# Performance work log

Hardware: AMD Instinct MI355X
Metric: run time of the kernel (lower is better)

## Reference

```python
import jax, jax.numpy as jnp
import numpy as np

D_MODEL = 1024
N_HEADS = 16
D_K = D_MODEL // N_HEADS
ROPE_BASE = 500000.0
RMS_EPS = 1e-10


def _rms_norm(x, w):
    # RMSNorm over last dim (per-head d_k): w * x / sqrt(mean(x^2) + eps)
    rms = jnp.sqrt(jnp.mean(x * x, axis=-1, keepdims=True) + RMS_EPS)
    return w * (x / rms)


def _rotate_half(x):
    x1, x2 = x[..., : x.shape[-1] // 2], x[..., x.shape[-1] // 2:]
    return jnp.concatenate([-x2, x1], axis=-1)


def _rope_cos_sin(seq_len):
    inv_freq = 1.0 / (ROPE_BASE ** (jnp.arange(0, D_K, 2, dtype=jnp.float32) / D_K))
    t = jnp.arange(seq_len, dtype=jnp.float32)
    freqs = jnp.outer(t, inv_freq)                # (S, d_k/2)
    emb = jnp.concatenate([freqs, freqs], axis=-1)  # (S, d_k)
    return jnp.cos(emb), jnp.sin(emb)


def setup_inputs() -> dict:
    key = jax.random.key(0)
    ks = jax.random.split(key, 9)
    B, S, D = 2, 2048, D_MODEL
    scale = 1.0 / np.sqrt(D)
    return {
        "q": jax.random.normal(ks[0], (B, S, D), jnp.float32),
        "k": jax.random.normal(ks[1], (B, S, D), jnp.float32),
        "v": jax.random.normal(ks[2], (B, S, D), jnp.float32),
        "w_q": jax.random.normal(ks[3], (D, D), jnp.float32) * scale,
        "w_k": jax.random.normal(ks[4], (D, D), jnp.float32) * scale,
        "w_v": jax.random.normal(ks[5], (D, D), jnp.float32) * scale,
        "w_o": jax.random.normal(ks[6], (D, D), jnp.float32) * scale,
        "q_norm_w": jnp.ones((D_K,), jnp.float32),
        "k_norm_w": jnp.ones((D_K,), jnp.float32),
    }


def reference(q, k, v, w_q, w_k, w_v, w_o, q_norm_w, k_norm_w):
    B, S, D = q.shape
    H, Dk = N_HEADS, D_K

    # QKV projections (nn.Linear without bias: x @ W.T), split into heads
    query = jnp.einsum("bsd,ed->bse", q, w_q).reshape(B, S, H, Dk).transpose(0, 2, 1, 3)
    key_ = jnp.einsum("bsd,ed->bse", k, w_k).reshape(B, S, H, Dk).transpose(0, 2, 1, 3)
    value = jnp.einsum("bsd,ed->bse", v, w_v).reshape(B, S, H, Dk).transpose(0, 2, 1, 3)

    # QK-norm (per-head RMSNorm)
    query = _rms_norm(query, q_norm_w)
    key_ = _rms_norm(key_, k_norm_w)

    # RoPE, default positions 0..S-1
    cos, sin = _rope_cos_sin(S)          # (S, d_k)
    cos = cos[None, None]                # (1,1,S,d_k)
    sin = sin[None, None]
    query = query * cos + _rotate_half(query) * sin
    key_ = key_ * cos + _rotate_half(key_) * sin

    # Causal scaled dot-product attention
    scale = 1.0 / jnp.sqrt(jnp.asarray(Dk, query.dtype))
    scores = jnp.einsum("bhqd,bhkd->bhqk", query, key_) * scale
    causal = jnp.tril(jnp.ones((S, S), dtype=bool))
    scores = jnp.where(causal, scores, jnp.finfo(scores.dtype).min)
    attn = jax.nn.softmax(scores, axis=-1)
    out = jnp.einsum("bhqk,bhkd->bhqd", attn, value)  # (B,H,S,d_k)

    out = out.transpose(0, 2, 1, 3).reshape(B, S, D)
    return jnp.einsum("bsd,ed->bse", out, w_o)
```

## Files before the change

### kernel.cpp

```cpp
#include <hip/hip_runtime.h>
#include <cstdint>
#include <cstddef>

typedef __bf16 bf16;
typedef __bf16 bf16x4_t __attribute__((ext_vector_type(4)));
typedef __bf16 bf16x8_t __attribute__((ext_vector_type(8)));
typedef float  f32x4_t  __attribute__((ext_vector_type(4)));

#define GLD_LDS16(g, l)                                                              \
  __builtin_amdgcn_global_load_lds((const __attribute__((address_space(1))) void*)(g), \
                                   (__attribute__((address_space(3))) void*)(l), 16, 0, 0)

#define S_WAITCNT_VMCNT(N) asm volatile("s_waitcnt vmcnt(" #N ")" ::: "memory")
#define S_BARRIER() asm volatile("s_barrier" ::: "memory")

__global__ __launch_bounds__(256) void cvt_kernel(
    const float* __restrict__ q, const float* __restrict__ k, const float* __restrict__ v,
    const float* __restrict__ wq, const float* __restrict__ wk, const float* __restrict__ wv,
    const float* __restrict__ wo,
    bf16* __restrict__ qb, bf16* __restrict__ kb, bf16* __restrict__ vb,
    bf16* __restrict__ wqb, bf16* __restrict__ wkb, bf16* __restrict__ wvb,
    bf16* __restrict__ wob)
{
  const float* src; bf16* dst; int n;
  switch (blockIdx.y) {
    case 0: src = q;  dst = qb;  n = 4194304; break;
    case 1: src = k;  dst = kb;  n = 4194304; break;
    case 2: src = v;  dst = vb;  n = 4194304; break;
    case 3: src = wq; dst = wqb; n = 1048576; break;
    case 4: src = wk; dst = wkb; n = 1048576; break;
    case 5: src = wv; dst = wvb; n = 1048576; break;
    default: src = wo; dst = wob; n = 1048576; break;
  }
  const int i = (blockIdx.x * 256 + threadIdx.x) * 4;
  if (i >= n) return;
  const float4 f = *(const float4*)(src + i);
  bf16x4_t o;
  o[0] = (bf16)f.x; o[1] = (bf16)f.y; o[2] = (bf16)f.z; o[3] = (bf16)f.w;
  *(bf16x4_t*)(dst + i) = o;
}

__device__ __forceinline__ void gemm_core(const bf16* __restrict__ A,
                                          const bf16* __restrict__ W,
                                          int m0, int n0, bf16* smem,
                                          f32x4_t (&acc)[4][4])
{
  const int K = 1024;
  bf16* As = smem;
  bf16* Bs = smem + 12288;
  const int t = threadIdx.x;
  const int lane = t & 63, w = t >> 6;
  const int l16 = lane & 15, qd = lane >> 4;
  const int wm = (w & 1) * 64, wn = (w >> 1) * 64;

  const int p8 = t >> 3;
  const int vslot = (t & 7) ^ (p8 & 7);
  const int srow = 2 * p8 + (vslot >> 2);
  const int scc = vslot & 3;
  const bf16* ag0 = A + (size_t)(m0 + srow) * K + scc * 8;
  const bf16* ag1 = A + (size_t)(m0 + 64 + srow) * K + scc * 8;
  const bf16* wg0 = W + (size_t)(n0 + srow) * K + scc * 8;
  const bf16* wg1 = W + (size_t)(n0 + 64 + srow) * K + scc * 8;
  const int lo0 = (w * 64) * 8;
  const int lo1 = (256 + w * 64) * 8;

  const int rslot = (((l16 & 1) * 4 + qd) ^ ((l16 >> 1) & 7)) * 8;
  const int abase = (wm >> 6) * 2048 + (l16 >> 1) * 64 + rslot;
  const int bbase = (wn >> 6) * 2048 + (l16 >> 1) * 64 + rslot;

#define STAGEG(k0_, b_)                                  \
  do {                                                   \
    GLD_LDS16(ag0 + (k0_), &As[(b_) * 4096 + lo0]);      \
    GLD_LDS16(ag1 + (k0_), &As[(b_) * 4096 + lo1]);      \
    GLD_LDS16(wg0 + (k0_), &Bs[(b_) * 4096 + lo0]);      \
    GLD_LDS16(wg1 + (k0_), &Bs[(b_) * 4096 + lo1]);      \
  } while (0)

  STAGEG(0, 0);
  STAGEG(32, 1);

  for (int k0 = 0; k0 < K; k0 += 32) {
    const int it = k0 >> 5;
    const int cb = it - (it / 3) * 3;
    if (k0 + 32 < K) S_WAITCNT_VMCNT(4); else S_WAITCNT_VMCNT(0);
    S_BARRIER();
    if (k0 + 64 < K) {
      const int nb = (it + 2) - ((it + 2) / 3) * 3;
      STAGEG(k0 + 64, nb);
    }
    bf16x8_t af[4], bfg[4];
#pragma unroll
    for (int i = 0; i < 4; ++i)
      af[i] = *(const bf16x8_t*)(&As[cb * 4096 + abase + i * 512]);
#pragma unroll
    for (int j = 0; j < 4; ++j)
      bfg[j] = *(const bf16x8_t*)(&Bs[cb * 4096 + bbase + j * 512]);
#pragma unroll
    for (int i = 0; i < 4; ++i)
#pragma unroll
      for (int j = 0; j < 4; ++j)
        acc[i][j] = __builtin_amdgcn_mfma_f32_16x16x32_bf16(af[i], bfg[j], acc[i][j], 0, 0, 0);
  }
#undef STAGEG
}

__global__ __launch_bounds__(512) void gemm_qkv(
    const bf16* __restrict__ qb, const bf16* __restrict__ wqb,
    const bf16* __restrict__ kb, const bf16* __restrict__ wkb,
    const bf16* __restrict__ vb, const bf16* __restrict__ wvb,
    const float* __restrict__ qnw, const float* __restrict__ knw,
    bf16* __restrict__ Qp, bf16* __restrict__ Kp, bf16* __restrict__ Vt)
{
  __shared__ bf16 smem[49152];
  const int K = 1024;
  const int z = blockIdx.z;
  const bf16 *A, *W;
  if (z == 0)      { A = qb; W = wqb; }
  else if (z == 1) { A = kb; W = wkb; }
  else             { A = vb; W = wvb; }

  const int m0 = blockIdx.y * 256, n0 = blockIdx.x * 256;
  const int t = threadIdx.x;
  const int lane = t & 63, w = t >> 6;
  const int l16 = lane & 15, qd = lane >> 4;
  const int wm = (w >> 2) * 128, wn = (w & 3) * 64;

  bf16* As = smem;
  bf16* Bs = smem + 24576;

  const int p8 = t >> 3;
  const int vslot = (t & 7) ^ (p8 & 7);
  const int srow = 2 * p8 + (vslot >> 2);
  const int scc = vslot & 3;
  const bf16* ag0 = A + (size_t)(m0 + srow) * K + scc * 8;
  const bf16* ag1 = A + (size_t)(m0 + 128 + srow) * K + scc * 8;
  const bf16* wg0 = W + (size_t)(n0 + srow) * K + scc * 8;
  const bf16* wg1 = W + (size_t)(n0 + 128 + srow) * K + scc * 8;
  const int lo0 = t * 8;
  const int lo1 = 4096 + t * 8;

  const int rslot = (((l16 & 1) * 4 + qd) ^ ((l16 >> 1) & 7)) * 8;
  const int abase = (w >> 2) * 4096 + (l16 >> 1) * 64 + rslot;
  const int bbase = ((w >> 1) & 1) * 4096 + ((w & 1) * 32 + (l16 >> 1)) * 64 + rslot;

  f32x4_t acc[8][4] = {};

#define STAGEG(k0_, b_)                                  \
  do {                                                   \
    GLD_LDS16(ag0 + (k0_), &As[(b_) * 8192 + lo0]);      \
    GLD_LDS16(ag1 + (k0_), &As[(b_) * 8192 + lo1]);      \
    GLD_LDS16(wg0 + (k0_), &Bs[(b_) * 8192 + lo0]);      \
    GLD_LDS16(wg1 + (k0_), &Bs[(b_) * 8192 + lo1]);      \
  } while (0)

  STAGEG(0, 0);
  STAGEG(32, 1);

  for (int kk = 0; kk < 32; ++kk) {
    const int cb = kk - (kk / 3) * 3;
    if (kk < 31) S_WAITCNT_VMCNT(4); else S_WAITCNT_VMCNT(0);
    S_BARRIER();
    if (kk + 2 < 32) {
      const int nb = (kk + 2) - ((kk + 2) / 3) * 3;
      STAGEG((kk + 2) * 32, nb);
    }
    bf16x8_t af[8], bfg[4];
#pragma unroll
    for (int i = 0; i < 8; ++i)
      af[i] = *(const bf16x8_t*)(&As[cb * 8192 + abase + i * 512]);
#pragma unroll
    for (int j = 0; j < 4; ++j)
      bfg[j] = *(const bf16x8_t*)(&Bs[cb * 8192 + bbase + j * 512]);
#pragma unroll
    for (int i = 0; i < 8; ++i)
#pragma unroll
      for (int j = 0; j < 4; ++j)
        acc[i][j] = __builtin_amdgcn_mfma_f32_16x16x32_bf16(af[i], bfg[j], acc[i][j], 0, 0, 0);
  }
#undef STAGEG

  const int h = blockIdx.x * 4 + (w & 3);
  const int b = (m0 + wm) >> 11;

  if (z == 2) {
#pragma unroll
    for (int i = 0; i < 8; ++i) {
      const int sq = ((m0 + wm) & 2047) + i * 16 + qd * 4;
      const int pos = (sq & ~31) + 8 * qd + 4 * (i & 1);
#pragma unroll
      for (int j = 0; j < 4; ++j) {
        const int dk = j * 16 + l16;
        bf16x4_t ov;
#pragma unroll
        for (int r = 0; r < 4; ++r) ov[r] = (bf16)acc[i][j][r];
        *(bf16x4_t*)(Vt + ((size_t)((b * 16 + h) * 64 + dk)) * 2048 + pos) = ov;
      }
    }
    return;
  }

  const float* nw = (z == 0) ? qnw : knw;
  const float osc = (z == 0) ? 0.125f * 1.44269504088896f : 1.0f;
  bf16* Out = (z == 0) ? Qp : Kp;

  float nwv[4];
#pragma unroll
  for (int j = 0; j < 4; ++j) nwv[j] = nw[j * 16 + l16];
  float invf[2];
#pragma unroll
  for (int jj = 0; jj < 2; ++jj) {
    const int d = jj * 16 + l16;
    invf[jj] = __builtin_amdgcn_exp2f(-(float)(2 * d) * (18.93156857f / 64.0f)) * 0.15915494309f;
  }

  __syncthreads();
  bf16* ep = smem + w * 1152;

#pragma unroll
  for (int i = 0; i < 8; ++i) {
    const int sbase = ((m0 + wm) & 2047) + i * 16 + qd * 4;
    float ssq[4];
#pragma unroll
    for (int r = 0; r < 4; ++r) {
      ssq[r] = 0.f;
#pragma unroll
      for (int j = 0; j < 4; ++j) ssq[r] += acc[i][j][r] * acc[i][j][r];
    }
#pragma unroll
    for (int off = 1; off < 16; off <<= 1)
#pragma unroll
      for (int r = 0; r < 4; ++r) ssq[r] += __shfl_xor(ssq[r], off);

    float xn[4][4];
#pragma unroll
    for (int r = 0; r < 4; ++r) {
      const float inv = 1.0f / sqrtf(ssq[r] * (1.0f / 64.0f) + 1e-10f);
#pragma unroll
      for (int j = 0; j < 4; ++j) xn[j][r] = acc[i][j][r] * inv * nwv[j];
    }
#pragma unroll
    for (int jj = 0; jj < 2; ++jj) {
#pragma unroll
      for (int r = 0; r < 4; ++r) {
        const int s = sbase + r;
        float rev = (float)s * invf[jj];
        rev = rev - floorf(rev);
        const float cv = __builtin_amdgcn_cosf(rev);
        const float sv = __builtin_amdgcn_sinf(rev);
        const float o1 = (xn[jj][r] * cv - xn[jj + 2][r] * sv) * osc;
        const float o2 = (xn[jj + 2][r] * cv + xn[jj][r] * sv) * osc;
        const int prow = qd * 4 + r;
        ep[prow * 72 + jj * 16 + l16] = (bf16)o1;
        ep[prow * 72 + 32 + jj * 16 + l16] = (bf16)o2;
      }
    }
    const int sg = ((m0 + wm) & 2047) + i * 16 + l16;
    const bf16x8_t t0 = *(const bf16x8_t*)(ep + l16 * 72 + qd * 16);
    const bf16x8_t t1 = *(const bf16x8_t*)(ep + l16 * 72 + qd * 16 + 8);
    bf16* gb = Out + ((size_t)(b * 16 + h) * 2048 + sg) * 64 + qd * 16;
    *(bf16x8_t*)(gb) = t0;
    *(bf16x8_t*)(gb + 8) = t1;
  }
}

__global__ __launch_bounds__(256) void gemm_out_k(
    const bf16* __restrict__ Ob, const bf16* __restrict__ wob, float* __restrict__ out)
{
  __shared__ bf16 smem[24576];
  const int N = 1024;

  const int orig = blockIdx.x + 8 * blockIdx.y;
  const int wgid = (orig & 7) * 32 + (orig >> 3);
  const int by = wgid >> 3, bx = wgid & 7;

  const int m0 = by * 128, n0 = bx * 128;
  f32x4_t acc[4][4] = {};
  gemm_core(Ob, wob, m0, n0, smem, acc);

  const int t = threadIdx.x;
  const int lane = t & 63, w = t >> 6;
  const int l16 = lane & 15, qd = lane >> 4;
  const int wm = (w & 1) * 64, wn = (w >> 1) * 64;

  __syncthreads();
  float* epf = (float*)smem + w * 1088;

#pragma unroll
  for (int i = 0; i < 4; ++i) {
#pragma unroll
    for (int j = 0; j < 4; ++j)
#pragma unroll
      for (int r = 0; r < 4; ++r)
        epf[(qd * 4 + r) * 68 + j * 16 + l16] = acc[i][j][r];
    const int row = m0 + wm + i * 16 + l16;
#pragma unroll
    for (int c = 0; c < 4; ++c) {
      const f32x4_t vv = *(const f32x4_t*)(epf + l16 * 68 + qd * 16 + c * 4);
      *(f32x4_t*)(out + (size_t)row * N + n0 + wn + qd * 16 + c * 4) = vv;
    }
  }
}

__global__ __launch_bounds__(512) void flash_attn(
    const bf16* __restrict__ Qp, const bf16* __restrict__ Kp,
    const bf16* __restrict__ Vt, bf16* __restrict__ O)
{
  const int S = 2048;

  const int orig = blockIdx.x + 16 * blockIdx.y;
  const int wgid = (orig & 7) * 64 + (orig >> 3);
  const int bx = wgid & 15, bh = wgid >> 4;

  const int qt = 15 - bx;
  const int t = threadIdx.x;
  const int lane = t & 63, w = t >> 6;
  const int l16 = lane & 15, qd = lane >> 4;

  __shared__ bf16 Ks[3][64 * 64];
  __shared__ bf16 Vs[3][64 * 64];

  const int qrow = qt * 128 + w * 16 + l16;
  const bf16* qbase = Qp + ((size_t)bh * S + qrow) * 64 + qd * 8;
  const bf16x8_t qf0 = *(const bf16x8_t*)qbase;
  const bf16x8_t qf1 = *(const bf16x8_t*)(qbase + 32);

  f32x4_t o_acc[4] = {};
  float l_i = 0.f;

  const int srow = t >> 3;
  const int scol = ((t & 7) ^ (srow & 7)) * 8;
  const bf16* kg = Kp + ((size_t)bh * S + srow) * 64 + scol;
  const bf16* vg = Vt + ((size_t)(bh * 64 + srow)) * S + scol;
  const int lo = w * 512;

  const int sw = l16 & 7;

#define STAGE(kt_, b_)                                 \
  do {                                                 \
    GLD_LDS16(kg + (size_t)(kt_) * 4096, &Ks[b_][lo]); \
    GLD_LDS16(vg + (kt_) * 64, &Vs[b_][lo]);           \
  } while (0)

  const int ktmax = 2 * qt + 1;
  STAGE(0, 0);
  STAGE(1, 1);

  for (int kt = 0; kt <= ktmax; ++kt) {
    const int cb = kt - (kt / 3) * 3;
    if (kt < ktmax) S_WAITCNT_VMCNT(2); else S_WAITCNT_VMCNT(0);
    S_BARRIER();
    if (kt + 2 <= ktmax) {
      const int nb = (kt + 2) - ((kt + 2) / 3) * 3;
      STAGE(kt + 2, nb);
    }

    if (kt == ktmax && w < 4) continue;

    f32x4_t sf[4];
    __builtin_amdgcn_s_setprio(1);
#pragma unroll
    for (int nt = 0; nt < 4; ++nt) {
      sf[nt][0] = -12.f; sf[nt][1] = -12.f; sf[nt][2] = -12.f; sf[nt][3] = -12.f;
      const bf16x8_t kf0 = *(const bf16x8_t*)(&Ks[cb][(nt * 16 + l16) * 64 + ((0 + qd) ^ sw) * 8]);
      const bf16x8_t kf1 = *(const bf16x8_t*)(&Ks[cb][(nt * 16 + l16) * 64 + ((4 + qd) ^ sw) * 8]);
      sf[nt] = __builtin_amdgcn_mfma_f32_16x16x32_bf16(kf0, qf0, sf[nt], 0, 0, 0);
      sf[nt] = __builtin_amdgcn_mfma_f32_16x16x32_bf16(kf1, qf1, sf[nt], 0, 0, 0);
    }
    __builtin_amdgcn_s_setprio(0);

    if (kt >= ktmax - 1) {
      const int kofs = (kt - 2 * qt) * 64;
      const int q_local = w * 16 + l16;
#pragma unroll
      for (int nt = 0; nt < 4; ++nt)
#pragma unroll
        for (int r = 0; r < 4; ++r)
          if (kofs + nt * 16 + qd * 4 + r > q_local) sf[nt][r] = -100.f;
    }

    bf16x4_t pb[4];
#pragma unroll
    for (int nt = 0; nt < 4; ++nt)
#pragma unroll
      for (int r = 0; r < 4; ++r) {
        const float p = __builtin_amdgcn_exp2f(sf[nt][r]);
        l_i += p;
        pb[nt][r] = (bf16)p;
      }

    __builtin_amdgcn_s_setprio(1);
#pragma unroll
    for (int nt2 = 0; nt2 < 2; ++nt2) {
      bf16x8_t pf;
#pragma unroll
      for (int r = 0; r < 4; ++r) { pf[r] = pb[2 * nt2][r]; pf[4 + r] = pb[2 * nt2 + 1][r]; }
#pragma unroll
      for (int dt = 0; dt < 4; ++dt) {
        const int row = dt * 16 + l16;
        const bf16x8_t vf =
            *(const bf16x8_t*)(&Vs[cb][row * 64 + ((4 * nt2 + qd) ^ sw) * 8]);
        o_acc[dt] = __builtin_amdgcn_mfma_f32_16x16x32_bf16(vf, pf, o_acc[dt], 0, 0, 0);
      }
    }
    __builtin_amdgcn_s_setprio(0);
  }
#undef STAGE

  l_i += __shfl_xor(l_i, 16);
  l_i += __shfl_xor(l_i, 32);

  const int b = bh >> 4, h = bh & 15;
  const float inv_l = 1.0f / l_i;
  const int qg = qt * 128 + w * 16 + l16;
#pragma unroll
  for (int dt = 0; dt < 4; ++dt) {
    bf16x4_t ov;
#pragma unroll
    for (int r = 0; r < 4; ++r) ov[r] = (bf16)(o_acc[dt][r] * inv_l);
    *(bf16x4_t*)(O + ((size_t)(b * S + qg)) * 1024 + h * 64 + dt * 16 + qd * 4) = ov;
  }
}

extern "C" void kernel_launch(void* const* d_in, const int* in_sizes, int n_in,
                              void* d_out, int out_size, void* d_ws, size_t ws_size,
                              hipStream_t stream)
{
  const float* q   = (const float*)d_in[0];
  const float* k   = (const float*)d_in[1];
  const float* v   = (const float*)d_in[2];
  const float* wq  = (const float*)d_in[3];
  const float* wk  = (const float*)d_in[4];
  const float* wv  = (const float*)d_in[5];
  const float* wo  = (const float*)d_in[6];
  const float* qnw = (const float*)d_in[7];
  const float* knw = (const float*)d_in[8];

  char* ws = (char*)d_ws;
  const size_t MB = 1u << 20;
  bf16* qb  = (bf16*)(ws + 0 * MB);
  bf16* kb  = (bf16*)(ws + 8 * MB);
  bf16* vb  = (bf16*)(ws + 16 * MB);
  bf16* wqb = (bf16*)(ws + 24 * MB);
  bf16* wkb = (bf16*)(ws + 26 * MB);
  bf16* wvb = (bf16*)(ws + 28 * MB);
  bf16* wob = (bf16*)(ws + 30 * MB);
  bf16* Qp  = (bf16*)(ws + 32 * MB);
  bf16* Kp  = (bf16*)(ws + 40 * MB);
  bf16* Vtr = (bf16*)(ws + 48 * MB);
  bf16* Oattn = qb;

  cvt_kernel<<<dim3(4096, 7), 256, 0, stream>>>(q, k, v, wq, wk, wv, wo,
                                                qb, kb, vb, wqb, wkb, wvb, wob);
  gemm_qkv<<<dim3(4, 16, 3), 512, 0, stream>>>(qb, wqb, kb, wkb, vb, wvb,
                                               qnw, knw, Qp, Kp, Vtr);
  flash_attn<<<dim3(16, 32), 512, 0, stream>>>(Qp, Kp, Vtr, Oattn);
  gemm_out_k<<<dim3(8, 32), 256, 0, stream>>>(Oattn, wob, (float*)d_out);
}
```

Before: 212.5 us.

## Fuse fp32-to-bf16 activation conversion into QKV GEMM A-tile loading

The separate conversion pass over the q/k/v activations is removed. The QKV GEMM now loads fp32 activations straight into registers, converts them to bf16 and writes them to LDS one stage ahead, while the weights keep the async global-to-LDS path. This drops a full write and re-read of 24MB of bf16 activations and trims the conversion kernel to weights only. In exchange the A tile is staged through registers, with extra register pressure, LDS write waits and fp32 global traffic inside the GEMM pipeline.

```diff
diff --git a/kernel.cpp b/kernel.cpp
--- a/kernel.cpp
+++ b/kernel.cpp
@@ -12,28 +12,23 @@
                                    (__attribute__((address_space(3))) void*)(l), 16, 0, 0)
 
 #define S_WAITCNT_VMCNT(N) asm volatile("s_waitcnt vmcnt(" #N ")" ::: "memory")
+#define S_WAITCNT_LGKM0()  asm volatile("s_waitcnt lgkmcnt(0)" ::: "memory")
 #define S_BARRIER() asm volatile("s_barrier" ::: "memory")
 
-__global__ __launch_bounds__(256) void cvt_kernel(
-    const float* __restrict__ q, const float* __restrict__ k, const float* __restrict__ v,
-    const float* __restrict__ wq, const float* __restrict__ wk, const float* __restrict__ wv,
-    const float* __restrict__ wo,
-    bf16* __restrict__ qb, bf16* __restrict__ kb, bf16* __restrict__ vb,
-    bf16* __restrict__ wqb, bf16* __restrict__ wkb, bf16* __restrict__ wvb,
-    bf16* __restrict__ wob)
-{
-  const float* src; bf16* dst; int n;
+__global__ __launch_bounds__(256) void cvt_w(
+    const float* __restrict__ wq, const float* __restrict__ wk,
+    const float* __restrict__ wv, const float* __restrict__ wo,
+    bf16* __restrict__ wqb, bf16* __restrict__ wkb,
+    bf16* __restrict__ wvb, bf16* __restrict__ wob)
+{
+  const float* src; bf16* dst;
   switch (blockIdx.y) {
-    case 0: src = q;  dst = qb;  n = 4194304; break;
-    case 1: src = k;  dst = kb;  n = 4194304; break;
-    case 2: src = v;  dst = vb;  n = 4194304; break;
-    case 3: src = wq; dst = wqb; n = 1048576; break;
-    case 4: src = wk; dst = wkb; n = 1048576; break;
-    case 5: src = wv; dst = wvb; n = 1048576; break;
-    default: src = wo; dst = wob; n = 1048576; break;
+    case 0:  src = wq; dst = wqb; break;
+    case 1:  src = wk; dst = wkb; break;
+    case 2:  src = wv; dst = wvb; break;
+    default: src = wo; dst = wob; break;
   }
   const int i = (blockIdx.x * 256 + threadIdx.x) * 4;
-  if (i >= n) return;
   const float4 f = *(const float4*)(src + i);
   bf16x4_t o;
   o[0] = (bf16)f.x; o[1] = (bf16)f.y; o[2] = (bf16)f.z; o[3] = (bf16)f.w;
@@ -105,19 +100,20 @@
 }
 
 __global__ __launch_bounds__(512) void gemm_qkv(
-    const bf16* __restrict__ qb, const bf16* __restrict__ wqb,
-    const bf16* __restrict__ kb, const bf16* __restrict__ wkb,
-    const bf16* __restrict__ vb, const bf16* __restrict__ wvb,
+    const float* __restrict__ qf, const bf16* __restrict__ wqb,
+    const float* __restrict__ kf, const bf16* __restrict__ wkb,
+    const float* __restrict__ vf, const bf16* __restrict__ wvb,
     const float* __restrict__ qnw, const float* __restrict__ knw,
     bf16* __restrict__ Qp, bf16* __restrict__ Kp, bf16* __restrict__ Vt)
 {
   __shared__ bf16 smem[49152];
   const int K = 1024;
   const int z = blockIdx.z;
-  const bf16 *A, *W;
-  if (z == 0)      { A = qb; W = wqb; }
-  else if (z == 1) { A = kb; W = wkb; }
-  else             { A = vb; W = wvb; }
+  const float* Af;
+  const bf16* W;
+  if (z == 0)      { Af = qf; W = wqb; }
+  else if (z == 1) { Af = kf; W = wkb; }
+  else             { Af = vf; W = wvb; }
 
   const int m0 = blockIdx.y * 256, n0 = blockIdx.x * 256;
   const int t = threadIdx.x;
@@ -132,8 +128,8 @@
   const int vslot = (t & 7) ^ (p8 & 7);
   const int srow = 2 * p8 + (vslot >> 2);
   const int scc = vslot & 3;
-  const bf16* ag0 = A + (size_t)(m0 + srow) * K + scc * 8;
-  const bf16* ag1 = A + (size_t)(m0 + 128 + srow) * K + scc * 8;
+  const float* agf0 = Af + (size_t)(m0 + srow) * K + scc * 8;
+  const float* agf1 = Af + (size_t)(m0 + 128 + srow) * K + scc * 8;
   const bf16* wg0 = W + (size_t)(n0 + srow) * K + scc * 8;
   const bf16* wg1 = W + (size_t)(n0 + 128 + srow) * K + scc * 8;
   const int lo0 = t * 8;
@@ -144,25 +140,58 @@
   const int bbase = ((w >> 1) & 1) * 4096 + ((w & 1) * 32 + (l16 >> 1)) * 64 + rslot;
 
   f32x4_t acc[8][4] = {};
-
-#define STAGEG(k0_, b_)                                  \
+  float4 pa0, pa1, pa2, pa3;
+
+#define AISSUE(k0_)                                   \
+  do {                                                \
+    pa0 = *(const float4*)(agf0 + (k0_));             \
+    pa1 = *(const float4*)(agf0 + (k0_) + 4);         \
+    pa2 = *(const float4*)(agf1 + (k0_));             \
+    pa3 = *(const float4*)(agf1 + (k0_) + 4);         \
+  } while (0)
+
+#define AWRITE(b_)                                                              \
+  do {                                                                          \
+    bf16x8_t h0, h1;                                                            \
+    h0[0] = (bf16)pa0.x; h0[1] = (bf16)pa0.y; h0[2] = (bf16)pa0.z;              \
+    h0[3] = (bf16)pa0.w; h0[4] = (bf16)pa1.x; h0[5] = (bf16)pa1.y;              \
+    h0[6] = (bf16)pa1.z; h0[7] = (bf16)pa1.w;                                   \
+    h1[0] = (bf16)pa2.x; h1[1] = (bf16)pa2.y; h1[2] = (bf16)pa2.z;              \
+    h1[3] = (bf16)pa2.w; h1[4] = (bf16)pa3.x; h1[5] = (bf16)pa3.y;              \
+    h1[6] = (bf16)pa3.z; h1[7] = (bf16)pa3.w;                                   \
+    *(bf16x8_t*)(&As[(b_) * 8192 + lo0]) = h0;                                  \
+    *(bf16x8_t*)(&As[(b_) * 8192 + lo1]) = h1;                                  \
+  } while (0)
+
+#define WISSUE(k0_, b_)                                  \
   do {                                                   \
-    GLD_LDS16(ag0 + (k0_), &As[(b_) * 8192 + lo0]);      \
-    GLD_LDS16(ag1 + (k0_), &As[(b_) * 8192 + lo1]);      \
     GLD_LDS16(wg0 + (k0_), &Bs[(b_) * 8192 + lo0]);      \
     GLD_LDS16(wg1 + (k0_), &Bs[(b_) * 8192 + lo1]);      \
   } while (0)
 
-  STAGEG(0, 0);
-  STAGEG(32, 1);
+  AISSUE(0);
+  S_WAITCNT_VMCNT(0);
+  AWRITE(0);
+  __builtin_amdgcn_sched_barrier(0);
+  AISSUE(32);
+  __builtin_amdgcn_sched_barrier(0);
+  WISSUE(0, 0);
+  WISSUE(32, 1);
 
   for (int kk = 0; kk < 32; ++kk) {
     const int cb = kk - (kk / 3) * 3;
-    if (kk < 31) S_WAITCNT_VMCNT(4); else S_WAITCNT_VMCNT(0);
+    if (kk < 31) S_WAITCNT_VMCNT(2); else S_WAITCNT_VMCNT(0);
+    if (kk < 31) {
+      const int wb = (kk + 1) - ((kk + 1) / 3) * 3;
+      AWRITE(wb);
+    }
+    S_WAITCNT_LGKM0();
     S_BARRIER();
-    if (kk + 2 < 32) {
+    if (kk < 30) {
       const int nb = (kk + 2) - ((kk + 2) / 3) * 3;
-      STAGEG((kk + 2) * 32, nb);
+      AISSUE((kk + 2) * 32);
+      __builtin_amdgcn_sched_barrier(0);
+      WISSUE((kk + 2) * 32, nb);
     }
     bf16x8_t af[8], bfg[4];
 #pragma unroll
@@ -177,7 +206,9 @@
       for (int j = 0; j < 4; ++j)
         acc[i][j] = __builtin_amdgcn_mfma_f32_16x16x32_bf16(af[i], bfg[j], acc[i][j], 0, 0, 0);
   }
-#undef STAGEG
+#undef AISSUE
+#undef AWRITE
+#undef WISSUE
 
   const int h = blockIdx.x * 4 + (w & 3);
   const int b = (m0 + wm) >> 11;
@@ -437,9 +468,6 @@
 
   char* ws = (char*)d_ws;
   const size_t MB = 1u << 20;
-  bf16* qb  = (bf16*)(ws + 0 * MB);
-  bf16* kb  = (bf16*)(ws + 8 * MB);
-  bf16* vb  = (bf16*)(ws + 16 * MB);
   bf16* wqb = (bf16*)(ws + 24 * MB);
   bf16* wkb = (bf16*)(ws + 26 * MB);
   bf16* wvb = (bf16*)(ws + 28 * MB);
@@ -447,11 +475,10 @@
   bf16* Qp  = (bf16*)(ws + 32 * MB);
   bf16* Kp  = (bf16*)(ws + 40 * MB);
   bf16* Vtr = (bf16*)(ws + 48 * MB);
-  bf16* Oattn = qb;
-
-  cvt_kernel<<<dim3(4096, 7), 256, 0, stream>>>(q, k, v, wq, wk, wv, wo,
-                                                qb, kb, vb, wqb, wkb, wvb, wob);
-  gemm_qkv<<<dim3(4, 16, 3), 512, 0, stream>>>(qb, wqb, kb, wkb, vb, wvb,
+  bf16* Oattn = (bf16*)(ws + 0 * MB);
+
+  cvt_w<<<dim3(1024, 4), 256, 0, stream>>>(wq, wk, wv, wo, wqb, wkb, wvb, wob);
+  gemm_qkv<<<dim3(4, 16, 3), 512, 0, stream>>>(q, wqb, k, wkb, v, wvb,
                                                qnw, knw, Qp, Kp, Vtr);
   flash_attn<<<dim3(16, 32), 512, 0, stream>>>(Qp, Kp, Vtr, Oattn);
   gemm_out_k<<<dim3(8, 32), 256, 0, stream>>>(Oattn, wob, (float*)d_out);
```

Result: slower. 217.8 us (+2.5%).
